# Performance work log

Hardware: AMD Instinct MI355X
Metric: run time of the kernel (lower is better)

## Reference

```python
import jax, jax.numpy as jnp
import numpy as np

N_NODES = 50000
N_EDGES = 1600000
IN_CH = 128
OUT_CH = 64
HEADS = 2
NEG_SLOPE = 0.2


def setup_inputs() -> dict:
    key = jax.random.key(0)
    ks = jax.random.split(key, 9)
    return {
        "x": jax.random.normal(ks[0], (N_NODES, IN_CH), dtype=jnp.float32),
        "embedding": jax.random.normal(ks[1], (N_NODES, OUT_CH), dtype=jnp.float32),
        "lin_w": jax.random.normal(ks[2], (IN_CH, HEADS * OUT_CH), dtype=jnp.float32) * (1.0 / np.sqrt(IN_CH)),
        "att_i": jax.random.normal(ks[3], (HEADS, OUT_CH), dtype=jnp.float32) * 0.1,
        "att_j": jax.random.normal(ks[4], (HEADS, OUT_CH), dtype=jnp.float32) * 0.1,
        "att_em_i": jax.random.normal(ks[5], (HEADS, OUT_CH), dtype=jnp.float32) * 0.1,
        "att_em_j": jax.random.normal(ks[6], (HEADS, OUT_CH), dtype=jnp.float32) * 0.1,
        "edge_src": jax.random.randint(ks[7], (N_EDGES,), 0, N_NODES, dtype=jnp.int64 if jax.config.read("jax_enable_x64") else jnp.int32),
        "edge_dst": jax.random.randint(ks[8], (N_EDGES,), 0, N_NODES, dtype=jnp.int64 if jax.config.read("jax_enable_x64") else jnp.int32),
    }


def reference(x, embedding, lin_w, att_i, att_j, att_em_i, att_em_j, edge_src, edge_dst):
    N = x.shape[0]
    H, D = att_i.shape
    # linear projection: [N, H, D]
    xh = (x @ lin_w).reshape(N, H, D)
    # add self loops
    loop = jnp.arange(N, dtype=edge_src.dtype)
    src = jnp.concatenate([edge_src, loop])
    dst = jnp.concatenate([edge_dst, loop])
    # per-node attention scores (cat(x, emb) . cat(att, att_em) split into two dots)
    s_i = jnp.einsum("nhd,hd->nh", xh, att_i) + embedding @ att_em_i.T  # [N,H]
    s_j = jnp.einsum("nhd,hd->nh", xh, att_j) + embedding @ att_em_j.T  # [N,H]
    # per-edge attention: x_i is src feature, x_j is dst feature (as in source)
    alpha = jax.nn.leaky_relu(s_i[src] + s_j[dst], negative_slope=NEG_SLOPE)  # [E+N,H]
    alpha = jax.nn.softmax(alpha, axis=1)  # softmax over heads, per the source code
    # message is alpha * x[dst]; aggregated at dst => x[n] * sum of alpha over incoming edges
    w = jax.ops.segment_sum(alpha, dst, num_segments=N)  # [N,H]
    out = xh * w[:, :, None]  # [N,H,D]
    return out.mean(axis=1)  # [N,D]
```

## Files before the change

### kernel.cpp

```cpp
#include <hip/hip_runtime.h>
#include <hip/hip_bf16.h>

#define IN_CH 128
#define OUT_CH 64
#define NEG_SLOPE 0.2f
#define KPACK 1024.5f

#define BSHIFT 8
#define CHUNK 4096
#define NGEMM 391
#define CAPMAX 9216
#define FIX20 1048576.0f

typedef short bf16x8 __attribute__((ext_vector_type(8)));
typedef float f32x4 __attribute__((ext_vector_type(4)));
typedef unsigned long long u64;
typedef unsigned int u32;

__device__ __forceinline__ unsigned short f2bf(float f) {
  union { float f; unsigned u; } v;
  v.f = f;
  unsigned r = v.u + 0x7FFF + ((v.u >> 16) & 1);
  return (unsigned short)(r >> 16);
}

__global__ __launch_bounds__(256) void prep_kernel(
    const float* __restrict__ lw, const float* __restrict__ att_i,
    const float* __restrict__ att_j, unsigned short* __restrict__ lwt,
    float* __restrict__ u, int* __restrict__ gcur) {
  const int bid = blockIdx.x;
  const int tid = threadIdx.x;
  if (bid == 0) gcur[tid] = 0;
  if (bid < 64) {
    int idx = bid * 256 + tid;
    int k = idx >> 7;
    int c = idx & 127;
    lwt[(size_t)c * IN_CH + k] = f2bf(lw[idx]);
  } else {
    int which = bid - 64;
    const float* att = which ? att_j : att_i;
    int k = tid & 127;
    int h = (tid >> 7) & 1;
    float v = 0.f;
#pragma unroll 8
    for (int d = 0; d < 64; ++d)
      v = fmaf(lw[(size_t)k * IN_CH + h * 64 + d], att[h * 64 + d], v);
    u[which * 256 + h * 128 + k] = v;
  }
}

__global__ __launch_bounds__(256) void score_kernel(
    const float* __restrict__ x, const float* __restrict__ emb,
    const float* __restrict__ u, const float* __restrict__ aei,
    const float* __restrict__ aej, float2* __restrict__ si,
    float2* __restrict__ sj, float* __restrict__ wself,
    float* __restrict__ wsum, int N) {
  const int tid = threadIdx.x;
  const int wave = tid >> 6;
  const int lane = tid & 63;
  const int n = blockIdx.x * 4 + wave;
  if (n >= N) return;

  float x0 = x[(size_t)n * IN_CH + lane];
  float x1 = x[(size_t)n * IN_CH + 64 + lane];
  float em = emb[(size_t)n * OUT_CH + lane];

  float v_si0 = fmaf(x0, u[lane], fmaf(x1, u[64 + lane], em * aei[lane]));
  float v_si1 =
      fmaf(x0, u[128 + lane], fmaf(x1, u[192 + lane], em * aei[64 + lane]));
  float v_sj0 =
      fmaf(x0, u[256 + lane], fmaf(x1, u[320 + lane], em * aej[lane]));
  float v_sj1 =
      fmaf(x0, u[384 + lane], fmaf(x1, u[448 + lane], em * aej[64 + lane]));

#pragma unroll
  for (int off = 32; off > 0; off >>= 1) {
    v_si0 += __shfl_xor(v_si0, off, 64);
    v_si1 += __shfl_xor(v_si1, off, 64);
    v_sj0 += __shfl_xor(v_sj0, off, 64);
    v_sj1 += __shfl_xor(v_sj1, off, 64);
  }

  if (lane == 0) {
    si[n] = make_float2(v_si0, v_si1);
    sj[n] = make_float2(v_sj0, v_sj1);
    float a0 = v_si0 + v_sj0;
    float a1 = v_si1 + v_sj1;
    a0 = a0 > 0.f ? a0 : NEG_SLOPE * a0;
    a1 = a1 > 0.f ? a1 : NEG_SLOPE * a1;
    wself[n] = 1.f / (1.f + __expf(a1 - a0));
    wsum[n] = 0.f;
  }
}

__global__ __launch_bounds__(256) void bin_gemm_kernel(
    const float* __restrict__ x, const unsigned short* __restrict__ lwt,
    const int* __restrict__ esrc, const int* __restrict__ edst,
    const float2* __restrict__ si, const float2* __restrict__ sj,
    float* __restrict__ xh, float* __restrict__ wsum,
    u32* __restrict__ brecs, int* __restrict__ gcur, int cap, int nbin, int N,
    int E) {
  __shared__ u32 recs[CHUNK];
  __shared__ int hist[256];
  __shared__ int scan[256];
  __shared__ int gbase[256];
  __shared__ int cur[256];
  const int bid = blockIdx.x;
  const int tid = threadIdx.x;
  const int wave = tid >> 6;
  const int lane = tid & 63;

  if (bid < nbin) {
    hist[tid] = 0;
    __syncthreads();

    const long e0 = (long)bid * CHUNK;
    const int cnt = (int)min((long)CHUNK, (long)E - e0);

    for (int r = tid; r < cnt; r += 256)
      atomicAdd(&hist[edst[e0 + r] >> BSHIFT], 1);
    __syncthreads();

    scan[tid] = hist[tid];
    __syncthreads();
#pragma unroll
    for (int ofs = 1; ofs < 256; ofs <<= 1) {
      int t = (tid >= ofs) ? scan[tid - ofs] : 0;
      __syncthreads();
      scan[tid] += t;
      __syncthreads();
    }
    int excl = scan[tid] - hist[tid];
    __syncthreads();
    scan[tid] = excl;
    cur[tid] = excl;
    gbase[tid] = (hist[tid] > 0) ? atomicAdd(&gcur[tid], hist[tid]) : 0;
    __syncthreads();

    for (int r = tid; r < cnt; r += 256) {
      long e = e0 + r;
      int s = esrc[e];
      int d = edst[e];
      float2 aa = si[s];
      float2 bb = sj[d];
      float a0 = aa.x + bb.x;
      float a1 = aa.y + bb.y;
      a0 = a0 > 0.f ? a0 : NEG_SLOPE * a0;
      a1 = a1 > 0.f ? a1 : NEG_SLOPE * a1;
      float p0 = 1.f / (1.f + __expf(a1 - a0));
      u32 fx = (u32)fminf(p0 * FIX20 + 0.5f, 1048575.0f);
      int pos = atomicAdd(&cur[d >> BSHIFT], 1);
      recs[pos] = ((u32)(d & 255) << 20) | fx;
    }
    __syncthreads();

    for (int p = tid; p < cnt; p += 256) {
      int lo = 0, hi = 255;
#pragma unroll
      for (int it = 0; it < 8; ++it) {
        int mid = (lo + hi + 1) >> 1;
        if (scan[mid] <= p) lo = mid; else hi = mid - 1;
      }
      int b = lo;
      int gofs = gbase[b] + (p - scan[b]);
      u32 rec = recs[p];
      if (gofs < cap) {
        brecs[(size_t)b * cap + gofs] = rec;
      } else {
        float p0 = (float)(rec & 0xFFFFF) * (1.0f / FIX20);
        unsafeAtomicAdd(&wsum[(b << BSHIFT) + (int)(rec >> 20)], KPACK + p0);
      }
    }
  } else {
    const int g = bid - nbin;
    const int ntiles = (N + 63) / 64;
    const int ko = (lane >> 4) * 8;
    const int ccol = lane & 15;
    for (int tile = g; tile < ntiles; tile += NGEMM) {
      const int row0 = tile * 64 + wave * 16;
      int arow = row0 + (lane & 15);
      if (arow >= N) arow = N - 1;
      const float* ap = x + (size_t)arow * IN_CH + ko;
      bf16x8 a[4];
#pragma unroll
      for (int kb = 0; kb < 4; ++kb) {
        float4 f0 = *(const float4*)(ap + kb * 32);
        float4 f1 = *(const float4*)(ap + kb * 32 + 4);
        bf16x8 t;
        t[0] = (short)f2bf(f0.x); t[1] = (short)f2bf(f0.y);
        t[2] = (short)f2bf(f0.z); t[3] = (short)f2bf(f0.w);
        t[4] = (short)f2bf(f1.x); t[5] = (short)f2bf(f1.y);
        t[6] = (short)f2bf(f1.z); t[7] = (short)f2bf(f1.w);
        a[kb] = t;
      }
      const int crow0 = row0 + (lane >> 4) * 4;
#pragma unroll
      for (int nt = 0; nt < 8; ++nt) {
        f32x4 acc = {0.f, 0.f, 0.f, 0.f};
        const bf16x8* bp =
            (const bf16x8*)(lwt + (size_t)(nt * 16 + ccol) * IN_CH + ko);
        acc = __builtin_amdgcn_mfma_f32_16x16x32_bf16(a[0], bp[0], acc, 0, 0, 0);
        acc = __builtin_amdgcn_mfma_f32_16x16x32_bf16(a[1], bp[4], acc, 0, 0, 0);
        acc = __builtin_amdgcn_mfma_f32_16x16x32_bf16(a[2], bp[8], acc, 0, 0, 0);
        acc = __builtin_amdgcn_mfma_f32_16x16x32_bf16(a[3], bp[12], acc, 0, 0, 0);
#pragma unroll
        for (int rr = 0; rr < 4; ++rr) {
          int n = crow0 + rr;
          if (n < N) xh[(size_t)n * IN_CH + nt * 16 + ccol] = acc[rr];
        }
      }
    }
  }
}

__global__ __launch_bounds__(1024) void reduce_out_kernel(
    const float* __restrict__ xh, const float* __restrict__ wsum,
    const float* __restrict__ wself, const u32* __restrict__ brecs,
    const int* __restrict__ gcur, int cap, float* __restrict__ out, int N) {
  __shared__ u64 table[256];
  const int b = blockIdx.x;
  const int tid = threadIdx.x;

  if (tid < 256) table[tid] = 0ull;
  __syncthreads();

  const int cnt = min(gcur[b], cap);
  const u32* rp = brecs + (size_t)b * cap;
  for (int r = tid; r < cnt; r += 1024) {
    u32 rec = rp[r];
    atomicAdd(&table[rec >> 20], (1ull << 32) | (u64)(rec & 0xFFFFF));
  }
  __syncthreads();

  const int n0 = b << BSHIFT;
  const int nmax = min(256, N - n0);
  for (int t = tid; t < nmax * 16; t += 1024) {
    int ln = t >> 4;
    int n = n0 + ln;
    int c4 = (t & 15) << 2;
    u64 acc = table[ln];
    float cnt_i = (float)(u32)(acc >> 32);
    float s0_i = (float)(u32)(acc & 0xFFFFFFFFu) * (1.0f / FIX20);
    float wsv = wsum[n];
    float cnt_s = floorf(wsv * (1.0f / KPACK));
    float s0_s = wsv - KPACK * cnt_s;
    float p0s = wself[n];
    float w0 = s0_i + s0_s + p0s;
    float w1 = (cnt_i + cnt_s - s0_i - s0_s) + (1.f - p0s);
    float4 v0 = *(const float4*)&xh[(size_t)n * IN_CH + c4];
    float4 v1 = *(const float4*)&xh[(size_t)n * IN_CH + 64 + c4];
    float4 o;
    o.x = 0.5f * fmaf(v0.x, w0, v1.x * w1);
    o.y = 0.5f * fmaf(v0.y, w0, v1.y * w1);
    o.z = 0.5f * fmaf(v0.z, w0, v1.z * w1);
    o.w = 0.5f * fmaf(v0.w, w0, v1.w * w1);
    *(float4*)&out[(size_t)n * OUT_CH + c4] = o;
  }
}

extern "C" void kernel_launch(void* const* d_in, const int* in_sizes, int n_in,
                              void* d_out, int out_size, void* d_ws,
                              size_t ws_size, hipStream_t stream) {
  const float* x = (const float*)d_in[0];
  const float* emb = (const float*)d_in[1];
  const float* lw = (const float*)d_in[2];
  const float* att_i = (const float*)d_in[3];
  const float* att_j = (const float*)d_in[4];
  const float* aei = (const float*)d_in[5];
  const float* aej = (const float*)d_in[6];
  const int* esrc = (const int*)d_in[7];
  const int* edst = (const int*)d_in[8];
  float* out = (float*)d_out;

  int N = in_sizes[0] / IN_CH;
  int E = in_sizes[7];
  int nb = (N + 255) >> BSHIFT;
  int nbin = (E + CHUNK - 1) / CHUNK;

  char* ws = (char*)d_ws;
  float* xh = (float*)ws;
  float2* si = (float2*)(ws + (size_t)N * IN_CH * 4);
  float2* sj = si + N;
  float* wself = (float*)(sj + N);
  float* wsum = wself + N;
  float* u = wsum + N;
  unsigned short* lwt = (unsigned short*)(u + 512);
  int* gcur = (int*)(lwt + 16384);
  u32* brecs = (u32*)(gcur + 256);

  size_t fixed = (size_t)((char*)brecs - ws);
  size_t avail = ws_size > fixed ? (ws_size - fixed) / 4 : 0;
  int cap = (int)(avail / (nb > 0 ? nb : 1));
  if (cap > CAPMAX) cap = CAPMAX;
  if (cap < 1024) cap = 1024;

  prep_kernel<<<dim3(66), dim3(256), 0, stream>>>(lw, att_i, att_j, lwt, u,
                                                  gcur);
  score_kernel<<<dim3((N + 3) / 4), dim3(256), 0, stream>>>(
      x, emb, u, aei, aej, si, sj, wself, wsum, N);
  bin_gemm_kernel<<<dim3(nbin + NGEMM), dim3(256), 0, stream>>>(
      x, lwt, esrc, edst, si, sj, xh, wsum, brecs, gcur, cap, nbin, N, E);
  reduce_out_kernel<<<dim3(nb), dim3(1024), 0, stream>>>(
      xh, wsum, wself, brecs, gcur, cap, out, N);
}
```

Measured before the change: 165.5 us.

## Replace binned edge aggregation with direct 64-bit atomics and fuse GEMM into output

Drops the shared-memory binning, scan and record buffers in favour of a simple edge kernel. Each thread handles four edges with nontemporal vector index loads and does one packed 64-bit global atomic per edge (count and fixed-point probability) straight into per-node slots. The projection GEMM is moved into a final kernel that applies the per-node head weights in registers and writes the output directly, so the xh intermediate is never written to or read back from memory. The cost is heavy contention on 1.6M random global 64-bit atomics, and the GEMM no longer overlaps with the edge work.

```diff
diff --git a/kernel.cpp b/kernel.cpp
--- a/kernel.cpp
+++ b/kernel.cpp
@@ -1,19 +1,13 @@
 #include <hip/hip_runtime.h>
-#include <hip/hip_bf16.h>
 
 #define IN_CH 128
 #define OUT_CH 64
 #define NEG_SLOPE 0.2f
-#define KPACK 1024.5f
-
-#define BSHIFT 8
-#define CHUNK 4096
-#define NGEMM 391
-#define CAPMAX 9216
 #define FIX20 1048576.0f
 
 typedef short bf16x8 __attribute__((ext_vector_type(8)));
 typedef float f32x4 __attribute__((ext_vector_type(4)));
+typedef int i32x4 __attribute__((ext_vector_type(4)));
 typedef unsigned long long u64;
 typedef unsigned int u32;
 
@@ -27,10 +21,9 @@
 __global__ __launch_bounds__(256) void prep_kernel(
     const float* __restrict__ lw, const float* __restrict__ att_i,
     const float* __restrict__ att_j, unsigned short* __restrict__ lwt,
-    float* __restrict__ u, int* __restrict__ gcur) {
+    float* __restrict__ u) {
   const int bid = blockIdx.x;
   const int tid = threadIdx.x;
-  if (bid == 0) gcur[tid] = 0;
   if (bid < 64) {
     int idx = bid * 256 + tid;
     int k = idx >> 7;
@@ -54,7 +47,7 @@
     const float* __restrict__ u, const float* __restrict__ aei,
     const float* __restrict__ aej, float2* __restrict__ si,
     float2* __restrict__ sj, float* __restrict__ wself,
-    float* __restrict__ wsum, int N) {
+    u64* __restrict__ wsum64, int N) {
   const int tid = threadIdx.x;
   const int wave = tid >> 6;
   const int lane = tid & 63;
@@ -89,56 +82,37 @@
     a0 = a0 > 0.f ? a0 : NEG_SLOPE * a0;
     a1 = a1 > 0.f ? a1 : NEG_SLOPE * a1;
     wself[n] = 1.f / (1.f + __expf(a1 - a0));
-    wsum[n] = 0.f;
-  }
-}
-
-__global__ __launch_bounds__(256) void bin_gemm_kernel(
-    const float* __restrict__ x, const unsigned short* __restrict__ lwt,
+    wsum64[n] = 0ull;
+  }
+}
+
+__global__ __launch_bounds__(256) void edge_kernel(
     const int* __restrict__ esrc, const int* __restrict__ edst,
     const float2* __restrict__ si, const float2* __restrict__ sj,
-    float* __restrict__ xh, float* __restrict__ wsum,
-    u32* __restrict__ brecs, int* __restrict__ gcur, int cap, int nbin, int N,
-    int E) {
-  __shared__ u32 recs[CHUNK];
-  __shared__ int hist[256];
-  __shared__ int scan[256];
-  __shared__ int gbase[256];
-  __shared__ int cur[256];
-  const int bid = blockIdx.x;
-  const int tid = threadIdx.x;
-  const int wave = tid >> 6;
-  const int lane = tid & 63;
-
-  if (bid < nbin) {
-    hist[tid] = 0;
-    __syncthreads();
-
-    const long e0 = (long)bid * CHUNK;
-    const int cnt = (int)min((long)CHUNK, (long)E - e0);
-
-    for (int r = tid; r < cnt; r += 256)
-      atomicAdd(&hist[edst[e0 + r] >> BSHIFT], 1);
-    __syncthreads();
-
-    scan[tid] = hist[tid];
-    __syncthreads();
-#pragma unroll
-    for (int ofs = 1; ofs < 256; ofs <<= 1) {
-      int t = (tid >= ofs) ? scan[tid - ofs] : 0;
-      __syncthreads();
-      scan[tid] += t;
-      __syncthreads();
-    }
-    int excl = scan[tid] - hist[tid];
-    __syncthreads();
-    scan[tid] = excl;
-    cur[tid] = excl;
-    gbase[tid] = (hist[tid] > 0) ? atomicAdd(&gcur[tid], hist[tid]) : 0;
-    __syncthreads();
-
-    for (int r = tid; r < cnt; r += 256) {
-      long e = e0 + r;
+    u64* __restrict__ wsum64, int E) {
+  const int t = blockIdx.x * 256 + threadIdx.x;
+  const long base = (long)t * 4;
+  if (base + 4 <= E) {
+    i32x4 s4 = __builtin_nontemporal_load((const i32x4*)(esrc + base));
+    i32x4 d4 = __builtin_nontemporal_load((const i32x4*)(edst + base));
+    float2 aa[4], bb[4];
+#pragma unroll
+    for (int k = 0; k < 4; ++k) {
+      aa[k] = si[s4[k]];
+      bb[k] = sj[d4[k]];
+    }
+#pragma unroll
+    for (int k = 0; k < 4; ++k) {
+      float a0 = aa[k].x + bb[k].x;
+      float a1 = aa[k].y + bb[k].y;
+      a0 = a0 > 0.f ? a0 : NEG_SLOPE * a0;
+      a1 = a1 > 0.f ? a1 : NEG_SLOPE * a1;
+      float p0 = 1.f / (1.f + __expf(a1 - a0));
+      u32 fx = (u32)fminf(p0 * FIX20 + 0.5f, 1048575.0f);
+      atomicAdd(&wsum64[d4[k]], (1ull << 32) | (u64)fx);
+    }
+  } else if (base < E) {
+    for (long e = base; e < E; ++e) {
       int s = esrc[e];
       int d = edst[e];
       float2 aa = si[s];
@@ -149,112 +123,74 @@
       a1 = a1 > 0.f ? a1 : NEG_SLOPE * a1;
       float p0 = 1.f / (1.f + __expf(a1 - a0));
       u32 fx = (u32)fminf(p0 * FIX20 + 0.5f, 1048575.0f);
-      int pos = atomicAdd(&cur[d >> BSHIFT], 1);
-      recs[pos] = ((u32)(d & 255) << 20) | fx;
-    }
-    __syncthreads();
-
-    for (int p = tid; p < cnt; p += 256) {
-      int lo = 0, hi = 255;
-#pragma unroll
-      for (int it = 0; it < 8; ++it) {
-        int mid = (lo + hi + 1) >> 1;
-        if (scan[mid] <= p) lo = mid; else hi = mid - 1;
-      }
-      int b = lo;
-      int gofs = gbase[b] + (p - scan[b]);
-      u32 rec = recs[p];
-      if (gofs < cap) {
-        brecs[(size_t)b * cap + gofs] = rec;
-      } else {
-        float p0 = (float)(rec & 0xFFFFF) * (1.0f / FIX20);
-        unsafeAtomicAdd(&wsum[(b << BSHIFT) + (int)(rec >> 20)], KPACK + p0);
-      }
-    }
-  } else {
-    const int g = bid - nbin;
-    const int ntiles = (N + 63) / 64;
-    const int ko = (lane >> 4) * 8;
-    const int ccol = lane & 15;
-    for (int tile = g; tile < ntiles; tile += NGEMM) {
-      const int row0 = tile * 64 + wave * 16;
-      int arow = row0 + (lane & 15);
-      if (arow >= N) arow = N - 1;
-      const float* ap = x + (size_t)arow * IN_CH + ko;
-      bf16x8 a[4];
-#pragma unroll
-      for (int kb = 0; kb < 4; ++kb) {
-        float4 f0 = *(const float4*)(ap + kb * 32);
-        float4 f1 = *(const float4*)(ap + kb * 32 + 4);
-        bf16x8 t;
-        t[0] = (short)f2bf(f0.x); t[1] = (short)f2bf(f0.y);
-        t[2] = (short)f2bf(f0.z); t[3] = (short)f2bf(f0.w);
-        t[4] = (short)f2bf(f1.x); t[5] = (short)f2bf(f1.y);
-        t[6] = (short)f2bf(f1.z); t[7] = (short)f2bf(f1.w);
-        a[kb] = t;
-      }
-      const int crow0 = row0 + (lane >> 4) * 4;
-#pragma unroll
-      for (int nt = 0; nt < 8; ++nt) {
-        f32x4 acc = {0.f, 0.f, 0.f, 0.f};
-        const bf16x8* bp =
-            (const bf16x8*)(lwt + (size_t)(nt * 16 + ccol) * IN_CH + ko);
-        acc = __builtin_amdgcn_mfma_f32_16x16x32_bf16(a[0], bp[0], acc, 0, 0, 0);
-        acc = __builtin_amdgcn_mfma_f32_16x16x32_bf16(a[1], bp[4], acc, 0, 0, 0);
-        acc = __builtin_amdgcn_mfma_f32_16x16x32_bf16(a[2], bp[8], acc, 0, 0, 0);
-        acc = __builtin_amdgcn_mfma_f32_16x16x32_bf16(a[3], bp[12], acc, 0, 0, 0);
-#pragma unroll
-        for (int rr = 0; rr < 4; ++rr) {
-          int n = crow0 + rr;
-          if (n < N) xh[(size_t)n * IN_CH + nt * 16 + ccol] = acc[rr];
-        }
-      }
-    }
-  }
-}
-
-__global__ __launch_bounds__(1024) void reduce_out_kernel(
-    const float* __restrict__ xh, const float* __restrict__ wsum,
-    const float* __restrict__ wself, const u32* __restrict__ brecs,
-    const int* __restrict__ gcur, int cap, float* __restrict__ out, int N) {
-  __shared__ u64 table[256];
-  const int b = blockIdx.x;
+      atomicAdd(&wsum64[d], (1ull << 32) | (u64)fx);
+    }
+  }
+}
+
+__global__ __launch_bounds__(256) void gemm_out_kernel(
+    const float* __restrict__ x, const unsigned short* __restrict__ lwt,
+    const u64* __restrict__ wsum64, const float* __restrict__ wself,
+    float* __restrict__ out, int N) {
   const int tid = threadIdx.x;
-
-  if (tid < 256) table[tid] = 0ull;
-  __syncthreads();
-
-  const int cnt = min(gcur[b], cap);
-  const u32* rp = brecs + (size_t)b * cap;
-  for (int r = tid; r < cnt; r += 1024) {
-    u32 rec = rp[r];
-    atomicAdd(&table[rec >> 20], (1ull << 32) | (u64)(rec & 0xFFFFF));
-  }
-  __syncthreads();
-
-  const int n0 = b << BSHIFT;
-  const int nmax = min(256, N - n0);
-  for (int t = tid; t < nmax * 16; t += 1024) {
-    int ln = t >> 4;
-    int n = n0 + ln;
-    int c4 = (t & 15) << 2;
-    u64 acc = table[ln];
-    float cnt_i = (float)(u32)(acc >> 32);
-    float s0_i = (float)(u32)(acc & 0xFFFFFFFFu) * (1.0f / FIX20);
-    float wsv = wsum[n];
-    float cnt_s = floorf(wsv * (1.0f / KPACK));
-    float s0_s = wsv - KPACK * cnt_s;
-    float p0s = wself[n];
-    float w0 = s0_i + s0_s + p0s;
-    float w1 = (cnt_i + cnt_s - s0_i - s0_s) + (1.f - p0s);
-    float4 v0 = *(const float4*)&xh[(size_t)n * IN_CH + c4];
-    float4 v1 = *(const float4*)&xh[(size_t)n * IN_CH + 64 + c4];
-    float4 o;
-    o.x = 0.5f * fmaf(v0.x, w0, v1.x * w1);
-    o.y = 0.5f * fmaf(v0.y, w0, v1.y * w1);
-    o.z = 0.5f * fmaf(v0.z, w0, v1.z * w1);
-    o.w = 0.5f * fmaf(v0.w, w0, v1.w * w1);
-    *(float4*)&out[(size_t)n * OUT_CH + c4] = o;
+  const int wave = tid >> 6;
+  const int lane = tid & 63;
+  const int ko = (lane >> 4) * 8;
+  const int ccol = lane & 15;
+  const int row0 = blockIdx.x * 64 + wave * 16;
+
+  int arow = row0 + (lane & 15);
+  if (arow >= N) arow = N - 1;
+  const float* ap = x + (size_t)arow * IN_CH + ko;
+  bf16x8 a[4];
+#pragma unroll
+  for (int kb = 0; kb < 4; ++kb) {
+    float4 f0 = *(const float4*)(ap + kb * 32);
+    float4 f1 = *(const float4*)(ap + kb * 32 + 4);
+    bf16x8 t;
+    t[0] = (short)f2bf(f0.x); t[1] = (short)f2bf(f0.y);
+    t[2] = (short)f2bf(f0.z); t[3] = (short)f2bf(f0.w);
+    t[4] = (short)f2bf(f1.x); t[5] = (short)f2bf(f1.y);
+    t[6] = (short)f2bf(f1.z); t[7] = (short)f2bf(f1.w);
+    a[kb] = t;
+  }
+
+  const int crow0 = row0 + (lane >> 4) * 4;
+  float w0r[4], w1r[4];
+#pragma unroll
+  for (int rr = 0; rr < 4; ++rr) {
+    int n = crow0 + rr;
+    if (n >= N) n = N - 1;
+    u64 acc = wsum64[n];
+    float cnt = (float)(u32)(acc >> 32);
+    float s0 = (float)(u32)(acc & 0xFFFFFFFFu) * (1.0f / FIX20);
+    float ps = wself[n];
+    w0r[rr] = 0.5f * (s0 + ps);
+    w1r[rr] = 0.5f * ((cnt - s0) + (1.f - ps));
+  }
+
+#pragma unroll
+  for (int nt = 0; nt < 4; ++nt) {
+    f32x4 acc0 = {0.f, 0.f, 0.f, 0.f};
+    f32x4 acc1 = {0.f, 0.f, 0.f, 0.f};
+    const bf16x8* bp0 =
+        (const bf16x8*)(lwt + (size_t)(nt * 16 + ccol) * IN_CH + ko);
+    const bf16x8* bp1 =
+        (const bf16x8*)(lwt + (size_t)(64 + nt * 16 + ccol) * IN_CH + ko);
+#pragma unroll
+    for (int kb = 0; kb < 4; ++kb) {
+      acc0 = __builtin_amdgcn_mfma_f32_16x16x32_bf16(a[kb], bp0[kb * 4], acc0,
+                                                     0, 0, 0);
+      acc1 = __builtin_amdgcn_mfma_f32_16x16x32_bf16(a[kb], bp1[kb * 4], acc1,
+                                                     0, 0, 0);
+    }
+#pragma unroll
+    for (int rr = 0; rr < 4; ++rr) {
+      int n = crow0 + rr;
+      if (n < N)
+        out[(size_t)n * OUT_CH + nt * 16 + ccol] =
+            fmaf(acc0[rr], w0r[rr], acc1[rr] * w1r[rr]);
+    }
   }
 }
 
@@ -274,32 +210,20 @@
 
   int N = in_sizes[0] / IN_CH;
   int E = in_sizes[7];
-  int nb = (N + 255) >> BSHIFT;
-  int nbin = (E + CHUNK - 1) / CHUNK;
 
   char* ws = (char*)d_ws;
-  float* xh = (float*)ws;
-  float2* si = (float2*)(ws + (size_t)N * IN_CH * 4);
+  u64* wsum64 = (u64*)ws;
+  float2* si = (float2*)(wsum64 + N);
   float2* sj = si + N;
   float* wself = (float*)(sj + N);
-  float* wsum = wself + N;
-  float* u = wsum + N;
+  float* u = wself + N;
   unsigned short* lwt = (unsigned short*)(u + 512);
-  int* gcur = (int*)(lwt + 16384);
-  u32* brecs = (u32*)(gcur + 256);
-
-  size_t fixed = (size_t)((char*)brecs - ws);
-  size_t avail = ws_size > fixed ? (ws_size - fixed) / 4 : 0;
-  int cap = (int)(avail / (nb > 0 ? nb : 1));
-  if (cap > CAPMAX) cap = CAPMAX;
-  if (cap < 1024) cap = 1024;
-
-  prep_kernel<<<dim3(66), dim3(256), 0, stream>>>(lw, att_i, att_j, lwt, u,
-                                                  gcur);
+
+  prep_kernel<<<dim3(66), dim3(256), 0, stream>>>(lw, att_i, att_j, lwt, u);
   score_kernel<<<dim3((N + 3) / 4), dim3(256), 0, stream>>>(
-      x, emb, u, aei, aej, si, sj, wself, wsum, N);
-  bin_gemm_kernel<<<dim3(nbin + NGEMM), dim3(256), 0, stream>>>(
-      x, lwt, esrc, edst, si, sj, xh, wsum, brecs, gcur, cap, nbin, N, E);
-  reduce_out_kernel<<<dim3(nb), dim3(1024), 0, stream>>>(
-      xh, wsum, wself, brecs, gcur, cap, out, N);
-}
+      x, emb, u, aei, aej, si, sj, wself, wsum64, N);
+  edge_kernel<<<dim3((E + 1023) / 1024), dim3(256), 0, stream>>>(
+      esrc, edst, si, sj, wsum64, E);
+  gemm_out_kernel<<<dim3((N + 63) / 64), dim3(256), 0, stream>>>(
+      x, lwt, wsum64, wself, out, N);
+}
```

Measured after the change: 214.8 us. 29.8% more time.
